# Kernel tuning notes

Hardware: AMD Instinct MI355X
Metric: run time of the kernel (lower is better)

Reference implementation:

```python
import jax, jax.numpy as jnp
import numpy as np

M = 100   # memory_size
D = 512   # memory_dim
B, C, H, W = 4, 512, 64, 64
LN_EPS = 512.0  # nn.LayerNorm(300, 512): 2nd positional arg is eps (faithful quirk)


def _l2norm(x):
    # F.normalize(x, dim=1): x / max(||x||_2, 1e-12)
    return x / jnp.maximum(jnp.linalg.norm(x, axis=1, keepdims=True), 1e-12)


def setup_inputs() -> dict:
    key = jax.random.key(0)
    ks = jax.random.split(key, 16)
    s = 0.03  # weight scale to keep activations sane
    return {
        "fea":    jax.random.normal(ks[0], (B, C, H, W), jnp.float32),
        "item_w": jax.random.normal(ks[1], (D, D), jnp.float32) * 0.02,
        "rel_w":  jax.random.normal(ks[2], (M, D, D), jnp.float32) * 0.02,
        "W1": jax.random.normal(ks[3], (C, D), jnp.float32) * s,  "b1": jnp.zeros((D,), jnp.float32),
        "W2": jax.random.normal(ks[4], (C, D), jnp.float32) * s,  "b2": jnp.zeros((D,), jnp.float32),
        "W3": jax.random.normal(ks[5], (C, M), jnp.float32) * s,  "b3": jnp.zeros((M,), jnp.float32),
        "Wqkv": jax.random.normal(ks[6], (D, 3 * M), jnp.float32) * s, "bqkv": jnp.zeros((3 * M,), jnp.float32),
        "ln_g": jnp.ones((3 * M,), jnp.float32), "ln_b": jnp.zeros((3 * M,), jnp.float32),
        "Wr1": jax.random.normal(ks[7], (D * D, D), jnp.float32) * s, "br1": jnp.zeros((D,), jnp.float32),
        "Wr2": jax.random.normal(ks[8], (M * D, D), jnp.float32) * s, "br2": jnp.zeros((D,), jnp.float32),
    }


def reference(fea, item_w, rel_w, W1, b1, W2, b2, W3, b3,
              Wqkv, bqkv, ln_g, ln_b, Wr1, br1, Wr2, br2):
    b, c, h, w = fea.shape
    x = fea.transpose(0, 2, 3, 1).reshape(b * h * w, c)        # (N, C)
    qn = _l2norm(x)
    ip1 = qn @ W1 + b1                                          # (N, D)
    ip2 = qn @ W2 + b2                                          # (N, D)
    ip3 = jax.nn.softmax(qn @ W3 + b3, axis=-1)                 # (N, M)
    # ip4[b,f] = sum_{n,d} ip3[b,n] ip2[b,d] rel_w[n,d,f]; scan over the M
    # memory slots to avoid an (N, M, D) intermediate.
    def _slot(acc, nw):
        coef, Wn = nw                                           # (N,), (D, D)
        return acc + coef[:, None] * (ip2 @ Wn), None
    ip4, _ = jax.lax.scan(_slot, jnp.zeros_like(ip2), (ip3.T, rel_w))
    # einsum('bd,cf->df', ip4, ip2) == outer(sum_b ip4, sum_c ip2)
    item0 = jnp.outer(ip4.sum(0), ip2.sum(0))                   # (D, D)
    item1 = item_w + ip1.T @ ip1                                # (D, D)
    qkv = (item0 + 1.0 * item1) @ Wqkv + bqkv                   # alpha2=1.0, (D, 3M)
    mu = qkv.mean(-1, keepdims=True)
    var = jnp.var(qkv, axis=-1, keepdims=True)                  # biased, as torch LN
    qkv = (qkv - mu) / jnp.sqrt(var + LN_EPS) * ln_g + ln_b
    q, k, v = qkv[:, :M].T, qkv[:, M:2 * M].T, qkv[:, 2 * M:].T  # each (M, D)
    # op_att: rel0[i,d,f] = sum_j tanh(q[i,d]*k[j,d]) * v[j,f]
    t = jnp.tanh(q[:, None, :] * k[None, :, :])                 # (M, M, D)
    rel0 = jnp.einsum('ijd,jf->idf', t, v)                      # (M, D, D)
    rel_w_new = rel_w + 1.0 * rel0                              # alpha1=1.0
    memory = rel_w_new.reshape(M, D * D) @ Wr1 + br1            # (M, D)
    mn = _l2norm(memory)
    addr = jax.nn.softmax(qn @ mn.T, axis=1)                    # (N, M)
    mf = (addr @ mn).reshape(b, h, w, c).transpose(0, 3, 1, 2)  # (b, C, h, w)
    return jnp.concatenate([fea, mf], axis=1)                   # (b, 2C, h, w)
```

## Files before the change

### kernel.cpp

```cpp
#include <hip/hip_runtime.h>
#include <hip/hip_bf16.h>

#define NTOK 16384
#define DDIM 512
#define MMEM 100
#define HWSZ 4096
#define QKVW 300

typedef __attribute__((ext_vector_type(8))) short short8v;
typedef __attribute__((ext_vector_type(4))) short short4v;
typedef __attribute__((ext_vector_type(4))) float f32x4;

__device__ __forceinline__ unsigned short f2bf(float x) {
  union { __hip_bfloat16 h; unsigned short u; } cv;
  cv.h = __float2bfloat16(x);
  return cv.u;
}
__device__ __forceinline__ float bf2f(unsigned short u) {
  union { unsigned int u; float f; } v; v.u = ((unsigned int)u) << 16;
  return v.f;
}

__global__ __launch_bounds__(256) void feat_cvtw_k(
    const float* __restrict__ fea, unsigned short* __restrict__ qnbf,
    float* __restrict__ out,
    const float* __restrict__ W1, const float* __restrict__ W2,
    const float* __restrict__ W3, const float* __restrict__ Wq,
    const float* __restrict__ b1, const float* __restrict__ b2,
    unsigned short* __restrict__ Wcat, unsigned short* __restrict__ o3,
    unsigned short* __restrict__ oq, float* __restrict__ bcat,
    float* __restrict__ zbase) {
  if (blockIdx.x >= 741) {
    int zidx = (blockIdx.x - 741) * 256 + threadIdx.x;
    if (zidx < 78592)
      ((float4*)zbase)[zidx] = make_float4(0.f, 0.f, 0.f, 0.f);
    return;
  }
  if (blockIdx.x >= 512) {
    int base = (blockIdx.x - 512) * 256 + threadIdx.x;
    for (int idx = base; idx < 467968; idx += 229 * 256) {
      if (idx < 262144) {
        int k = idx >> 9, n = idx & 511;
        Wcat[(size_t)k * 1024 + n] = f2bf(W1[idx]);
        Wcat[(size_t)k * 1024 + 512 + n] = f2bf(W2[idx]);
      } else if (idx < 313344) {
        o3[idx - 262144] = f2bf(W3[idx - 262144]);
      } else if (idx < 466944) {
        oq[idx - 313344] = f2bf(Wq[idx - 313344]);
      } else {
        int i = idx - 466944;
        bcat[i] = (i < 512) ? b1[i] : b2[i - 512];
      }
    }
    return;
  }
  __shared__ float tile[512][33];
  __shared__ float psum[8][32];
  __shared__ float invn_s[32];
  const int bid = blockIdx.x;
  const int b = bid >> 7, hw0 = (bid & 127) * 32;
  const int t = threadIdx.x;
  const int hwo = t & 31, cg = t >> 5;
  const float* src = fea + (size_t)b * DDIM * HWSZ + hw0;
  float* dst = out + (size_t)b * (2 * DDIM) * HWSZ + hw0;
  float ss = 0.f;
#pragma unroll 8
  for (int i = 0; i < 64; ++i) {
    int c = cg * 64 + i;
    float v = src[(size_t)c * HWSZ + hwo];
    tile[c][hwo] = v;
    dst[(size_t)c * HWSZ + hwo] = v;
    ss += v * v;
  }
  psum[cg][hwo] = ss;
  __syncthreads();
  if (t < 32) {
    float s = 0.f;
#pragma unroll
    for (int j = 0; j < 8; ++j) s += psum[j][t];
    invn_s[t] = 1.f / fmaxf(sqrtf(s), 1e-12f);
  }
  __syncthreads();
  const int tok = t & 31, c0 = (t >> 5) * 64;
  const float inv = invn_s[tok];
  unsigned short* qp = qnbf + ((size_t)(b * HWSZ + hw0 + tok)) * DDIM + c0;
#pragma unroll
  for (int e8 = 0; e8 < 8; ++e8) {
    short8v p;
#pragma unroll
    for (int e = 0; e < 8; ++e)
      p[e] = (short)f2bf(tile[c0 + e8 * 8 + e][tok] * inv);
    *(short8v*)(qp + e8 * 8) = p;
  }
}

__device__ __forceinline__ void gemm_body(
    char* smem, const unsigned short* __restrict__ A,
    const unsigned short* __restrict__ B, const float* __restrict__ bias,
    unsigned short* __restrict__ Cbf,
    int M, int N, int K, int lda, int ldb, int ldc, int bx, int by) {
  unsigned short (*As)[40] = (unsigned short(*)[40])smem;
  unsigned short (*Bs)[132] = (unsigned short(*)[132])(smem + 10240);
  const int tid = threadIdx.x;
  const int l = tid & 63, w = tid >> 6;
  const int l15 = l & 15, lhi = l >> 4;
  const int wm = w >> 1, wn = w & 1;
  const int row0 = by * 128, col0 = bx * 128;
  const int am = tid >> 1, akq = (tid & 1) << 4;
  const int bk = tid >> 3, bnq = (tid & 7) << 4;
  const int arow = row0 + am;
  f32x4 acc[4][4] = {};

  for (int k0 = 0; k0 < K; k0 += 32) {
    short8v av0 = {}, av1 = {}, bv0 = {}, bv1 = {};
    if (arow < M && k0 + akq < K) {
      const unsigned short* ap = A + (size_t)arow * lda + k0 + akq;
      if (k0 + akq + 15 < K) {
        av0 = *(const short8v*)ap;
        av1 = *(const short8v*)(ap + 8);
      } else {
#pragma unroll
        for (int e = 0; e < 8; ++e) {
          av0[e] = (k0 + akq + e < K) ? (short)ap[e] : (short)0;
          av1[e] = (k0 + akq + 8 + e < K) ? (short)ap[8 + e] : (short)0;
        }
      }
    }
    {
      const int kk = k0 + bk;
      if (kk < K) {
        const unsigned short* bp = B + (size_t)kk * ldb + col0 + bnq;
        if (col0 + bnq + 15 < N) {
          bv0 = *(const short8v*)bp;
          bv1 = *(const short8v*)(bp + 8);
        } else {
#pragma unroll
          for (int e = 0; e < 8; ++e) {
            bv0[e] = (col0 + bnq + e < N) ? (short)bp[e] : (short)0;
            bv1[e] = (col0 + bnq + 8 + e < N) ? (short)bp[8 + e] : (short)0;
          }
        }
      }
    }
    __syncthreads();
    *(short8v*)&As[am][akq] = av0;
    *(short8v*)&As[am][akq + 8] = av1;
    *(short8v*)&Bs[bk][bnq] = bv0;
    *(short8v*)&Bs[bk][bnq + 8] = bv1;
    __syncthreads();
    short8v af[4];
#pragma unroll
    for (int mt = 0; mt < 4; ++mt)
      af[mt] = *(const short8v*)&As[wm * 64 + mt * 16 + l15][lhi * 8];
#pragma unroll
    for (int ct = 0; ct < 4; ++ct) {
      union { short8v v; unsigned short u[8]; } bf;
      const int nn = wn * 64 + ct * 16 + l15;
#pragma unroll
      for (int j = 0; j < 8; ++j) bf.u[j] = Bs[lhi * 8 + j][nn];
#pragma unroll
      for (int mt = 0; mt < 4; ++mt)
        acc[mt][ct] = __builtin_amdgcn_mfma_f32_16x16x32_bf16(
            af[mt], bf.v, acc[mt][ct], 0, 0, 0);
    }
  }

#pragma unroll
  for (int mt = 0; mt < 4; ++mt) {
    const int rb = row0 + wm * 64 + mt * 16 + lhi * 4;
#pragma unroll
    for (int u = 0; u < 4; ++u) {
      const int r = rb + u;
      if (r >= M) continue;
#pragma unroll
      for (int ct = 0; ct < 4; ++ct) {
        const int c = col0 + wn * 64 + ct * 16 + l15;
        if (c >= N) continue;
        float val = acc[mt][ct][u];
        if (bias) val += bias[c];
        Cbf[(size_t)r * ldc + c] = f2bf(val);
      }
    }
  }
}

__device__ __forceinline__ void sm100_body(
    char* smem, const unsigned short* __restrict__ A,
    const unsigned short* __restrict__ B, const float* __restrict__ bias,
    unsigned short* __restrict__ obf, int lda, int ldb, int ldo, int rowblk) {
  unsigned short (*As)[40] = (unsigned short(*)[40])smem;
  unsigned short (*Bs)[132] = (unsigned short(*)[132])(smem + 10240);
  unsigned short (*Ps)[104] = (unsigned short(*)[104])smem;
  const int tid = threadIdx.x;
  const int l = tid & 63, w = tid >> 6;
  const int l15 = l & 15, lhi = l >> 4;
  const int wm = w >> 1, wn = w & 1;
  const int row0 = rowblk * 128;
  const int am = tid >> 1, akq = (tid & 1) << 4;
  const int bk = tid >> 3, bnq = (tid & 7) << 4;
  f32x4 acc[4][4] = {};

  for (int k0 = 0; k0 < DDIM; k0 += 32) {
    const unsigned short* ap = A + (size_t)(row0 + am) * lda + k0 + akq;
    short8v av0 = *(const short8v*)ap;
    short8v av1 = *(const short8v*)(ap + 8);
    short8v bv0 = {}, bv1 = {};
    const unsigned short* bp = B + (size_t)(k0 + bk) * ldb + bnq;
    if (bnq + 15 < MMEM) {
      bv0 = *(const short8v*)bp;
      bv1 = *(const short8v*)(bp + 8);
    } else {
#pragma unroll
      for (int e = 0; e < 8; ++e) {
        bv0[e] = (bnq + e < MMEM) ? (short)bp[e] : (short)0;
        bv1[e] = (bnq + 8 + e < MMEM) ? (short)bp[8 + e] : (short)0;
      }
    }
    __syncthreads();
    *(short8v*)&As[am][akq] = av0;
    *(short8v*)&As[am][akq + 8] = av1;
    *(short8v*)&Bs[bk][bnq] = bv0;
    *(short8v*)&Bs[bk][bnq + 8] = bv1;
    __syncthreads();
    short8v af[4];
#pragma unroll
    for (int mt = 0; mt < 4; ++mt)
      af[mt] = *(const short8v*)&As[wm * 64 + mt * 16 + l15][lhi * 8];
#pragma unroll
    for (int ct = 0; ct < 4; ++ct) {
      union { short8v v; unsigned short u[8]; } bf;
      const int nn = wn * 64 + ct * 16 + l15;
#pragma unroll
      for (int j = 0; j < 8; ++j) bf.u[j] = Bs[lhi * 8 + j][nn];
#pragma unroll
      for (int mt = 0; mt < 4; ++mt)
        acc[mt][ct] = __builtin_amdgcn_mfma_f32_16x16x32_bf16(
            af[mt], bf.v, acc[mt][ct], 0, 0, 0);
    }
  }

  __syncthreads();
#pragma unroll
  for (int mt = 0; mt < 4; ++mt) {
#pragma unroll
    for (int u = 0; u < 4; ++u) {
      const int r = wm * 64 + mt * 16 + lhi * 4 + u;
#pragma unroll
      for (int ct = 0; ct < 4; ++ct) {
        const int c = wn * 64 + ct * 16 + l15;
        if (c < MMEM) {
          float val = acc[mt][ct][u];
          if (bias) val += bias[c];
          Ps[r][c] = f2bf(val);
        }
      }
    }
  }
  __syncthreads();
  for (int rr = 0; rr < 32; ++rr) {
    const int r = w * 32 + rr;
    float v0 = bf2f(Ps[r][l]);
    const bool has1 = (l + 64) < MMEM;
    float v1 = has1 ? bf2f(Ps[r][l + 64]) : -3.4e38f;
    float m = fmaxf(v0, v1);
#pragma unroll
    for (int o = 32; o; o >>= 1) m = fmaxf(m, __shfl_xor(m, o, 64));
    float e0 = expf(v0 - m);
    float e1 = has1 ? expf(v1 - m) : 0.f;
    float s = e0 + e1;
#pragma unroll
    for (int o = 32; o; o >>= 1) s += __shfl_xor(s, o, 64);
    float inv = 1.f / s;
    unsigned short* orow = obf + (size_t)(row0 + r) * ldo;
    orow[l] = f2bf(e0 * inv);
    if (has1) orow[l + 64] = f2bf(e1 * inv);
  }
}

__device__ __forceinline__ void atb_body(
    char* smem, const unsigned short* __restrict__ A,
    const unsigned short* __restrict__ B, float* __restrict__ C,
    int M, int N, int K, int lda, int ldb, int ldc, int KC,
    int bx, int by, int bz) {
  unsigned short (*As)[40] = (unsigned short(*)[40])smem;
  unsigned short (*Bs)[132] = (unsigned short(*)[132])(smem + 10240);
  const int tid = threadIdx.x;
  const int l = tid & 63, w = tid >> 6;
  const int l15 = l & 15, lhi = l >> 4;
  const int wm = w >> 1, wn = w & 1;
  const int row0 = by * 128, col0 = bx * 128;
  const int kbeg = bz * KC;
  const int kend = min(kbeg + KC, K);
  const int akk = tid >> 3, amq = (tid & 7) << 4;
  const int bk = tid >> 3, bnq = (tid & 7) << 4;
  f32x4 acc[4][4] = {};

  for (int k0 = kbeg; k0 < kend; k0 += 32) {
    unsigned short av[16]; short8v bv0 = {}, bv1 = {};
    {
      const int kk = k0 + akk;
      if (kk < kend) {
        const unsigned short* ap = A + (size_t)kk * lda + row0 + amq;
        if (row0 + amq + 15 < M) {
          *(short8v*)&av[0] = *(const short8v*)ap;
          *(short8v*)&av[8] = *(const short8v*)(ap + 8);
        } else {
#pragma unroll
          for (int e = 0; e < 16; ++e)
            av[e] = (row0 + amq + e < M) ? ap[e] : 0;
        }
      } else {
#pragma unroll
        for (int e = 0; e < 16; ++e) av[e] = 0;
      }
    }
    {
      const int kk = k0 + bk;
      if (kk < kend) {
        const unsigned short* bp = B + (size_t)kk * ldb + col0 + bnq;
        if (col0 + bnq + 15 < N) {
          bv0 = *(const short8v*)bp;
          bv1 = *(const short8v*)(bp + 8);
        } else {
#pragma unroll
          for (int e = 0; e < 8; ++e) {
            bv0[e] = (col0 + bnq + e < N) ? (short)bp[e] : (short)0;
            bv1[e] = (col0 + bnq + 8 + e < N) ? (short)bp[8 + e] : (short)0;
          }
        }
      }
    }
    __syncthreads();
#pragma unroll
    for (int e = 0; e < 16; ++e) As[amq + e][akk] = av[e];
    *(short8v*)&Bs[bk][bnq] = bv0;
    *(short8v*)&Bs[bk][bnq + 8] = bv1;
    __syncthreads();
    short8v af[4];
#pragma unroll
    for (int mt = 0; mt < 4; ++mt)
      af[mt] = *(const short8v*)&As[wm * 64 + mt * 16 + l15][lhi * 8];
#pragma unroll
    for (int ct = 0; ct < 4; ++ct) {
      union { short8v v; unsigned short u[8]; } bf;
      const int nn = wn * 64 + ct * 16 + l15;
#pragma unroll
      for (int j = 0; j < 8; ++j) bf.u[j] = Bs[lhi * 8 + j][nn];
#pragma unroll
      for (int mt = 0; mt < 4; ++mt)
        acc[mt][ct] = __builtin_amdgcn_mfma_f32_16x16x32_bf16(
            af[mt], bf.v, acc[mt][ct], 0, 0, 0);
    }
  }

#pragma unroll
  for (int mt = 0; mt < 4; ++mt) {
    const int rb = row0 + wm * 64 + mt * 16 + lhi * 4;
#pragma unroll
    for (int u = 0; u < 4; ++u) {
      const int r = rb + u;
      if (r >= M) continue;
#pragma unroll
      for (int ct = 0; ct < 4; ++ct) {
        const int c = col0 + wn * 64 + ct * 16 + l15;
        if (c >= N) continue;
        atomicAdd(&C[(size_t)r * ldc + c], acc[mt][ct][u]);
      }
    }
  }
}

__global__ __launch_bounds__(256) void step2_k(
    const unsigned short* __restrict__ qnbf, const unsigned short* __restrict__ Wcat,
    const float* __restrict__ bcat, unsigned short* __restrict__ ip12bf,
    const unsigned short* __restrict__ W3bf, const float* __restrict__ b3,
    unsigned short* __restrict__ ip3bf) {
  __shared__ char smem[26624];
  const int bid = blockIdx.x;
  if (bid < 1024) {
    gemm_body(smem, qnbf, Wcat, bcat, ip12bf, NTOK, 1024, DDIM,
              DDIM, 1024, 1024, bid & 7, bid >> 3);
  } else {
    sm100_body(smem, qnbf, W3bf, b3, ip3bf, DDIM, MMEM, MMEM, bid - 1024);
  }
}

__global__ __launch_bounds__(256) void step3_k(
    const unsigned short* __restrict__ ip12bf, const unsigned short* __restrict__ ip3bf,
    float* __restrict__ item, float* __restrict__ S, float* __restrict__ ip2sum) {
  __shared__ char smem[18688];
  const int bid = blockIdx.x;
  const int t = threadIdx.x;
  if (bid < 512) {
    atb_body(smem, ip12bf, ip12bf, item, DDIM, DDIM, NTOK,
             1024, 1024, DDIM, 512, bid & 3, (bid >> 2) & 3, bid >> 4);
  } else if (bid < 768) {
    const int b2 = bid - 512;
    atb_body(smem, ip3bf, ip12bf + 512, S, MMEM, DDIM, NTOK,
             MMEM, 1024, DDIM, 256, b2 & 3, 0, b2 >> 2);
  } else {
    const int cb = bid - 768;
    const unsigned short* p = ip12bf + 512 + (size_t)cb * 64 * 1024 + t;
    float a0 = 0.f, a1 = 0.f, a2 = 0.f, a3 = 0.f;
    float b0 = 0.f, b1 = 0.f, b2 = 0.f, b3 = 0.f;
    for (int r = 0; r < 64; r += 4) {
      a0 += bf2f(p[(size_t)(r + 0) * 1024]); b0 += bf2f(p[(size_t)(r + 0) * 1024 + 256]);
      a1 += bf2f(p[(size_t)(r + 1) * 1024]); b1 += bf2f(p[(size_t)(r + 1) * 1024 + 256]);
      a2 += bf2f(p[(size_t)(r + 2) * 1024]); b2 += bf2f(p[(size_t)(r + 2) * 1024 + 256]);
      a3 += bf2f(p[(size_t)(r + 3) * 1024]); b3 += bf2f(p[(size_t)(r + 3) * 1024 + 256]);
    }
    atomicAdd(&ip2sum[t], (a0 + a1) + (a2 + a3));
    atomicAdd(&ip2sum[t + 256], (b0 + b1) + (b2 + b3));
  }
}

__global__ __launch_bounds__(256) void sm100_addr_k(
    const unsigned short* __restrict__ qnbf, const unsigned short* __restrict__ mnTbf,
    unsigned short* __restrict__ addrbf) {
  __shared__ char smem[26624];
  sm100_body(smem, qnbf, mnTbf, nullptr, addrbf, DDIM, MMEM, 128, blockIdx.x);
}

__global__ __launch_bounds__(256) void gemm_mf_out_k(
    const unsigned short* __restrict__ A, const unsigned short* __restrict__ B,
    float* __restrict__ out) {
  __shared__ char smem[35328];
  unsigned short (*As)[40] = (unsigned short(*)[40])smem;
  unsigned short (*Bs)[132] = (unsigned short(*)[132])(smem + 10240);
  unsigned short (*Ps)[138] = (unsigned short(*)[138])smem;
  const int tid = threadIdx.x;
  const int l = tid & 63, w = tid >> 6;
  const int l15 = l & 15, lhi = l >> 4;
  const int wm = w >> 1, wn = w & 1;
  const int row0 = blockIdx.y * 128, col0 = blockIdx.x * 128;
  const int am = tid >> 1, akq = (tid & 1) << 4;
  const int bk = tid >> 3, bnq = (tid & 7) << 4;
  const int K = MMEM, lda = 128, ldb = DDIM;
  f32x4 acc[4][4] = {};

  for (int k0 = 0; k0 < 128; k0 += 32) {
    short8v av0 = {}, av1 = {}, bv0 = {}, bv1 = {};
    if (k0 + akq < K) {
      const unsigned short* ap = A + (size_t)(row0 + am) * lda + k0 + akq;
      if (k0 + akq + 15 < K) {
        av0 = *(const short8v*)ap;
        av1 = *(const short8v*)(ap + 8);
      } else {
#pragma unroll
        for (int e = 0; e < 8; ++e) {
          av0[e] = (k0 + akq + e < K) ? (short)ap[e] : (short)0;
          av1[e] = (k0 + akq + 8 + e < K) ? (short)ap[8 + e] : (short)0;
        }
      }
    }
    {
      const int kk = k0 + bk;
      if (kk < K) {
        const unsigned short* bp = B + (size_t)kk * ldb + col0 + bnq;
        bv0 = *(const short8v*)bp;
        bv1 = *(const short8v*)(bp + 8);
      }
    }
    __syncthreads();
    *(short8v*)&As[am][akq] = av0;
    *(short8v*)&As[am][akq + 8] = av1;
    *(short8v*)&Bs[bk][bnq] = bv0;
    *(short8v*)&Bs[bk][bnq + 8] = bv1;
    __syncthreads();
    short8v af[4];
#pragma unroll
    for (int mt = 0; mt < 4; ++mt)
      af[mt] = *(const short8v*)&As[wm * 64 + mt * 16 + l15][lhi * 8];
#pragma unroll
    for (int ct = 0; ct < 4; ++ct) {
      union { short8v v; unsigned short u[8]; } bf;
      const int nn = wn * 64 + ct * 16 + l15;
#pragma unroll
      for (int j = 0; j < 8; ++j) bf.u[j] = Bs[lhi * 8 + j][nn];
#pragma unroll
      for (int mt = 0; mt < 4; ++mt)
        acc[mt][ct] = __builtin_amdgcn_mfma_f32_16x16x32_bf16(
            af[mt], bf.v, acc[mt][ct], 0, 0, 0);
    }
  }

  __syncthreads();
#pragma unroll
  for (int mt = 0; mt < 4; ++mt) {
#pragma unroll
    for (int u = 0; u < 4; ++u) {
      const int r = wm * 64 + mt * 16 + lhi * 4 + u;
#pragma unroll
      for (int ct = 0; ct < 4; ++ct) {
        const int c = wn * 64 + ct * 16 + l15;
        Ps[r][c] = f2bf(acc[mt][ct][u]);
      }
    }
  }
  __syncthreads();
  const int b = row0 >> 12;
  const int hwb = row0 & 4095;
  const int j = tid & 63;
  float* obase = out + (size_t)b * 4194304 + (size_t)(512 + col0) * HWSZ + hwb;
  for (int cr = tid >> 6; cr < 128; cr += 4) {
    obase[(size_t)cr * HWSZ + j]      = bf2f(Ps[j][cr]);
    obase[(size_t)cr * HWSZ + j + 64] = bf2f(Ps[j + 64][cr]);
  }
}

__global__ __launch_bounds__(256) void gemm_qkv_k(
    const float* __restrict__ item, const float* __restrict__ item_w,
    const float* __restrict__ s4, const float* __restrict__ s2,
    const unsigned short* __restrict__ B, const float* __restrict__ bias,
    float* __restrict__ C) {
  __shared__ unsigned short As[128][40];
  __shared__ unsigned short Bs[32][132];
  const int tid = threadIdx.x;
  const int l = tid & 63, w = tid >> 6;
  const int l15 = l & 15, lhi = l >> 4;
  const int wm = w >> 1, wn = w & 1;
  const int row0 = blockIdx.y * 128, col0 = blockIdx.x * 128;
  const int am = tid >> 1, akq = (tid & 1) << 4;
  const int bk = tid >> 3, bnq = (tid & 7) << 4;
  const int arow = row0 + am;
  f32x4 acc[4][4] = {};

  for (int k0 = 0; k0 < DDIM; k0 += 32) {
    float av[16];
    {
      const size_t off = (size_t)arow * DDIM + k0 + akq;
      const float s4r = s4[arow];
#pragma unroll
      for (int u = 0; u < 4; ++u) {
        float4 a = *(const float4*)(item + off + 4 * u);
        float4 b = *(const float4*)(item_w + off + 4 * u);
        float4 c = *(const float4*)(s2 + k0 + akq + 4 * u);
        av[4*u+0] = a.x + b.x + s4r * c.x;
        av[4*u+1] = a.y + b.y + s4r * c.y;
        av[4*u+2] = a.z + b.z + s4r * c.z;
        av[4*u+3] = a.w + b.w + s4r * c.w;
      }
    }
    short8v bv0 = {}, bv1 = {};
    {
      const int kk = k0 + bk;
      const unsigned short* bp = B + (size_t)kk * QKVW + col0 + bnq;
      if (col0 + bnq + 15 < QKVW) {
        bv0 = *(const short8v*)bp;
        bv1 = *(const short8v*)(bp + 8);
      } else {
#pragma unroll
        for (int e = 0; e < 8; ++e) {
          bv0[e] = (col0 + bnq + e < QKVW) ? (short)bp[e] : (short)0;
          bv1[e] = (col0 + bnq + 8 + e < QKVW) ? (short)bp[8 + e] : (short)0;
        }
      }
    }
    __syncthreads();
    {
      short8v p0, p1;
#pragma unroll
      for (int e = 0; e < 8; ++e) p0[e] = (short)f2bf(av[e]);
#pragma unroll
      for (int e = 0; e < 8; ++e) p1[e] = (short)f2bf(av[8 + e]);
      *(short8v*)&As[am][akq] = p0;
      *(short8v*)&As[am][akq + 8] = p1;
    }
    *(short8v*)&Bs[bk][bnq] = bv0;
    *(short8v*)&Bs[bk][bnq + 8] = bv1;
    __syncthreads();
    short8v af[4];
#pragma unroll
    for (int mt = 0; mt < 4; ++mt)
      af[mt] = *(const short8v*)&As[wm * 64 + mt * 16 + l15][lhi * 8];
#pragma unroll
    for (int ct = 0; ct < 4; ++ct) {
      union { short8v v; unsigned short u[8]; } bf;
      const int nn = wn * 64 + ct * 16 + l15;
#pragma unroll
      for (int j = 0; j < 8; ++j) bf.u[j] = Bs[lhi * 8 + j][nn];
#pragma unroll
      for (int mt = 0; mt < 4; ++mt)
        acc[mt][ct] = __builtin_amdgcn_mfma_f32_16x16x32_bf16(
            af[mt], bf.v, acc[mt][ct], 0, 0, 0);
    }
  }

#pragma unroll
  for (int mt = 0; mt < 4; ++mt) {
    const int rb = row0 + wm * 64 + mt * 16 + lhi * 4;
#pragma unroll
    for (int u = 0; u < 4; ++u) {
      const int r = rb + u;
#pragma unroll
      for (int ct = 0; ct < 4; ++ct) {
        const int c = col0 + wn * 64 + ct * 16 + l15;
        if (c >= QKVW) continue;
        C[(size_t)r * QKVW + c] = acc[mt][ct][u] + bias[c];
      }
    }
  }
}

__global__ __launch_bounds__(256) void rel0_mfma_k(
    const float* __restrict__ qm, const float* __restrict__ km,
    const float* __restrict__ vm, const float* __restrict__ rel_w,
    unsigned short* __restrict__ relbf) {
  __shared__ unsigned short Ts[128][136];
  __shared__ unsigned short Vs[128][136];
  __shared__ float qv[128];
  const int i = blockIdx.y;
  const int d0 = blockIdx.x * 128;
  const int tid = threadIdx.x;
  const int l = tid & 63, w = tid >> 6;
  const int l15 = l & 15, lhi = l >> 4;
  const int wm = w >> 1, wn = w & 1;

  if (tid < 128) qv[tid] = qm[(size_t)i * DDIM + d0 + tid];
  __syncthreads();
#pragma unroll
  for (int p = 0; p < 8; ++p) {
    int g = p * 2048 + tid * 8;
    int j = g >> 7, dd = g & 127;
    if (j < MMEM) {
      const float* kp = km + (size_t)j * DDIM + d0 + dd;
      float4 k0v = *(const float4*)kp;
      float4 k1v = *(const float4*)(kp + 4);
      float kv[8] = {k0v.x, k0v.y, k0v.z, k0v.w, k1v.x, k1v.y, k1v.z, k1v.w};
#pragma unroll
      for (int e = 0; e < 8; ++e)
        Ts[dd + e][j] = f2bf(tanhf(qv[dd + e] * kv[e]));
    } else {
#pragma unroll
      for (int e = 0; e < 8; ++e) Ts[dd + e][j] = 0;
    }
  }

  for (int f0 = 0; f0 < DDIM; f0 += 128) {
    __syncthreads();
#pragma unroll
    for (int p = 0; p < 8; ++p) {
      int g = p * 2048 + tid * 8;
      int j = g >> 7, ff = g & 127;
      short8v pv;
      if (j < MMEM) {
        const float* vp = vm + (size_t)j * DDIM + f0 + ff;
        float4 v0 = *(const float4*)vp;
        float4 v1 = *(const float4*)(vp + 4);
        pv[0] = (short)f2bf(v0.x); pv[1] = (short)f2bf(v0.y);
        pv[2] = (short)f2bf(v0.z); pv[3] = (short)f2bf(v0.w);
        pv[4] = (short)f2bf(v1.x); pv[5] = (short)f2bf(v1.y);
        pv[6] = (short)f2bf(v1.z); pv[7] = (short)f2bf(v1.w);
      } else {
#pragma unroll
        for (int e = 0; e < 8; ++e) pv[e] = 0;
      }
      *(short8v*)&Vs[j][ff] = pv;
    }
    __syncthreads();
    f32x4 acc[4][4] = {};
#pragma unroll
    for (int ks = 0; ks < 4; ++ks) {
      const int kb = ks * 32;
      short8v af[4];
#pragma unroll
      for (int mt = 0; mt < 4; ++mt)
        af[mt] = *(const short8v*)&Ts[wm * 64 + mt * 16 + l15][kb + lhi * 8];
#pragma unroll
      for (int ct = 0; ct < 4; ++ct) {
        union { short8v v; unsigned short u[8]; } bf;
        const int nn = wn * 64 + ct * 16 + l15;
#pragma unroll
        for (int jj = 0; jj < 8; ++jj) bf.u[jj] = Vs[kb + lhi * 8 + jj][nn];
#pragma unroll
        for (int mt = 0; mt < 4; ++mt)
          acc[mt][ct] = __builtin_amdgcn_mfma_f32_16x16x32_bf16(
              af[mt], bf.v, acc[mt][ct], 0, 0, 0);
      }
    }
#pragma unroll
    for (int mt = 0; mt < 4; ++mt) {
#pragma unroll
      for (int u = 0; u < 4; ++u) {
        const int d = d0 + wm * 64 + mt * 16 + lhi * 4 + u;
        const size_t base = (size_t)i * 262144 + (size_t)d * DDIM;
#pragma unroll
        for (int ct = 0; ct < 4; ++ct) {
          const int f = f0 + wn * 64 + ct * 16 + l15;
          relbf[base + f] = f2bf(rel_w[base + f] + acc[mt][ct][u]);
        }
      }
    }
  }
}

#define MGK 262144
#define MGKC 1024
#define MGCHUNK 256
__global__ __launch_bounds__(1024, 4) void memgemm_k(
    const unsigned short* __restrict__ Ag, const float* __restrict__ Bg,
    unsigned short* __restrict__ partial) {
  __shared__ unsigned short As[128][44];
  __shared__ unsigned short Bs[32][520];
  const int tid = threadIdx.x;
  const int l = tid & 63, w = tid >> 6;
  const int l15 = l & 15, lhi = l >> 4;
  const int kbeg = blockIdx.x * MGKC;
  const int arow = tid >> 3, akq = tid & 7;
  const int bk = tid >> 5, bnq = (tid & 31) * 16;
  const int bsw = ((bk >> 3) & 3) << 4;
  const int csw = lhi << 4;
  f32x4 acc[8][2] = {};

  for (int t32 = 0; t32 < MGKC / 32; ++t32) {
    const int kb = kbeg + t32 * 32;
    short4v av = {};
    if (arow < MMEM)
      av = *(const short4v*)(Ag + (size_t)arow * MGK + kb + akq * 4);
    float4 bv[4];
    const float* bp = Bg + (size_t)(kb + bk) * DDIM + bnq;
#pragma unroll
    for (int u = 0; u < 4; ++u) bv[u] = *(const float4*)(bp + 4 * u);
    __syncthreads();
    *(short4v*)&As[arow][akq * 4] = av;
#pragma unroll
    for (int u = 0; u < 2; ++u) {
      short8v pb;
      pb[0] = (short)f2bf(bv[2*u].x);   pb[1] = (short)f2bf(bv[2*u].y);
      pb[2] = (short)f2bf(bv[2*u].z);   pb[3] = (short)f2bf(bv[2*u].w);
      pb[4] = (short)f2bf(bv[2*u+1].x); pb[5] = (short)f2bf(bv[2*u+1].y);
      pb[6] = (short)f2bf(bv[2*u+1].z); pb[7] = (short)f2bf(bv[2*u+1].w);
      *(short8v*)&Bs[bk][(bnq + u * 8) ^ bsw] = pb;
    }
    __syncthreads();
    union { short8v v; unsigned short u[8]; } bf0, bf1;
    const int nn0 = w * 32 + l15, nn1 = w * 32 + 16 + l15;
#pragma unroll
    for (int j = 0; j < 8; ++j) {
      bf0.u[j] = Bs[lhi * 8 + j][nn0 ^ csw];
      bf1.u[j] = Bs[lhi * 8 + j][nn1 ^ csw];
    }
#pragma unroll
    for (int mt = 0; mt < 8; ++mt) {
      short8v af = *(const short8v*)&As[mt * 16 + l15][lhi * 8];
      acc[mt][0] = __builtin_amdgcn_mfma_f32_16x16x32_bf16(af, bf0.v, acc[mt][0], 0, 0, 0);
      acc[mt][1] = __builtin_amdgcn_mfma_f32_16x16x32_bf16(af, bf1.v, acc[mt][1], 0, 0, 0);
    }
  }

  unsigned short* pw = partial + (size_t)blockIdx.x * (MMEM * DDIM);
#pragma unroll
  for (int mt = 0; mt < 8; ++mt) {
    const int r0 = mt * 16 + lhi * 4;
#pragma unroll
    for (int r = 0; r < 4; ++r) {
      const int row = r0 + r;
      if (row < MMEM) {
        pw[(size_t)row * DDIM + w * 32 + l15]      = f2bf(acc[mt][0][r]);
        pw[(size_t)row * DDIM + w * 32 + 16 + l15] = f2bf(acc[mt][1][r]);
      }
    }
  }
}

__global__ __launch_bounds__(512) void reduce_mn_k(
    const unsigned short* __restrict__ partial, const float* __restrict__ br1,
    unsigned short* __restrict__ mnbf, unsigned short* __restrict__ mnTbf) {
  __shared__ float r1[8];
  const int i = blockIdx.x, t = threadIdx.x;
  const unsigned short* p = partial + (size_t)i * DDIM + t;
  float a[16] = {};
  const size_t zs = (size_t)(MMEM * DDIM);
  for (int z = 0; z < MGCHUNK; z += 16) {
#pragma unroll
    for (int e = 0; e < 16; ++e) a[e] += bf2f(p[(z + e) * zs]);
  }
  float s = br1[t];
#pragma unroll
  for (int e = 0; e < 16; ++e) s += a[e];
  float q = s * s;
#pragma unroll
  for (int o = 32; o; o >>= 1) q += __shfl_xor(q, o, 64);
  if ((t & 63) == 0) r1[t >> 6] = q;
  __syncthreads();
  q = 0.f;
#pragma unroll
  for (int j = 0; j < 8; ++j) q += r1[j];
  float inv = 1.f / fmaxf(sqrtf(q), 1e-12f);
  unsigned short hv = f2bf(s * inv);
  mnbf[(size_t)i * DDIM + t] = hv;
  mnTbf[(size_t)t * MMEM + i] = hv;
}

__global__ __launch_bounds__(256) void ip4sum_k(const float* __restrict__ S,
                                                const float* __restrict__ rel_w,
                                                float* __restrict__ out) {
  __shared__ float sv[64];
  int r0 = blockIdx.x * 64;
  int tid = threadIdx.x;
  if (tid < 64) sv[tid] = S[r0 + tid];
  __syncthreads();
  float a0 = 0.f, a1 = 0.f, a2 = 0.f, a3 = 0.f;
  float b0 = 0.f, b1 = 0.f, b2 = 0.f, b3 = 0.f;
  const float* base = rel_w + (size_t)r0 * DDIM;
  for (int r = 0; r < 64; r += 4) {
    const float* p0 = base + (size_t)(r + 0) * DDIM;
    const float* p1 = base + (size_t)(r + 1) * DDIM;
    const float* p2 = base + (size_t)(r + 2) * DDIM;
    const float* p3 = base + (size_t)(r + 3) * DDIM;
    a0 = fmaf(sv[r + 0], p0[tid], a0); b0 = fmaf(sv[r + 0], p0[tid + 256], b0);
    a1 = fmaf(sv[r + 1], p1[tid], a1); b1 = fmaf(sv[r + 1], p1[tid + 256], b1);
    a2 = fmaf(sv[r + 2], p2[tid], a2); b2 = fmaf(sv[r + 2], p2[tid + 256], b2);
    a3 = fmaf(sv[r + 3], p3[tid], a3); b3 = fmaf(sv[r + 3], p3[tid + 256], b3);
  }
  atomicAdd(&out[tid], (a0 + a1) + (a2 + a3));
  atomicAdd(&out[tid + 256], (b0 + b1) + (b2 + b3));
}

__global__ __launch_bounds__(256) void ln300_k(const float* __restrict__ x,
                                               const float* __restrict__ g,
                                               const float* __restrict__ bb,
                                               float* __restrict__ qm,
                                               float* __restrict__ km,
                                               float* __restrict__ vm) {
  __shared__ float r1[4], r2[4];
  int row = blockIdx.x, tid = threadIdx.x;
  const float* xr = x + (size_t)row * QKVW;
  float v1 = xr[tid];
  float v2 = (tid + 256 < QKVW) ? xr[tid + 256] : 0.f;
  float s = v1 + v2, q = v1 * v1 + v2 * v2;
#pragma unroll
  for (int o = 32; o; o >>= 1) { s += __shfl_xor(s, o, 64); q += __shfl_xor(q, o, 64); }
  if ((tid & 63) == 0) { r1[tid >> 6] = s; r2[tid >> 6] = q; }
  __syncthreads();
  s = r1[0] + r1[1] + r1[2] + r1[3];
  q = r2[0] + r2[1] + r2[2] + r2[3];
  float mean = s * (1.f / 300.f);
  float var = q * (1.f / 300.f) - mean * mean;
  float inv = rsqrtf(var + 512.0f);
  float y1 = (v1 - mean) * inv * g[tid] + bb[tid];
  int j = tid;
  if (j < 100)      qm[(size_t)j * DDIM + row] = y1;
  else if (j < 200) km[(size_t)(j - 100) * DDIM + row] = y1;
  else              vm[(size_t)(j - 200) * DDIM + row] = y1;
  if (tid + 256 < QKVW) {
    float y2 = (v2 - mean) * inv * g[tid + 256] + bb[tid + 256];
    vm[(size_t)(tid + 56) * DDIM + row] = y2;
  }
}

extern "C" void kernel_launch(void* const* d_in, const int* in_sizes, int n_in,
                              void* d_out, int out_size, void* d_ws, size_t ws_size,
                              hipStream_t stream) {
  (void)in_sizes; (void)n_in; (void)out_size; (void)ws_size;
  const float* fea    = (const float*)d_in[0];
  const float* item_w = (const float*)d_in[1];
  const float* rel_w  = (const float*)d_in[2];
  const float* W1     = (const float*)d_in[3];
  const float* b1     = (const float*)d_in[4];
  const float* W2     = (const float*)d_in[5];
  const float* b2     = (const float*)d_in[6];
  const float* W3     = (const float*)d_in[7];
  const float* b3     = (const float*)d_in[8];
  const float* Wqkv   = (const float*)d_in[9];
  const float* bqkv   = (const float*)d_in[10];
  const float* ln_g   = (const float*)d_in[11];
  const float* ln_b   = (const float*)d_in[12];
  const float* Wr1    = (const float*)d_in[13];
  const float* br1    = (const float*)d_in[14];
  float* out = (float*)d_out;
  float* ws = (float*)d_ws;

  float* S       = ws;
  float* ip4sum  = S       + 51200;
  float* ip2sum  = ip4sum  + 512;
  float* item    = ip2sum  + 512;
  float* qkv     = item    + 262144;
  float* qm      = qkv     + 153600;
  float* km      = qm      + 51200;
  float* vm      = km      + 51200;
  float* bcat    = vm      + 51200;
  unsigned short* u16base = (unsigned short*)(bcat + 1024);
  unsigned short* partial = u16base;
  unsigned short* qnbf    = partial + 13107200;
  unsigned short* ip12bf  = qnbf    + 8388608;
  unsigned short* ip3bf   = ip12bf  + 16777216;
  unsigned short* addrbf  = ip3bf   + 1638400;
  unsigned short* relbf   = addrbf  + 2097152;
  unsigned short* mnbf    = relbf   + 26214400;
  unsigned short* mnTbf   = mnbf    + 51200;
  unsigned short* Wcat    = mnTbf   + 51200;
  unsigned short* W3bf    = Wcat    + 524288;
  unsigned short* Wqbf    = W3bf    + 51200;

  feat_cvtw_k<<<1048, 256, 0, stream>>>(fea, qnbf, out, W1, W2, W3, Wqkv,
                                        b1, b2, Wcat, W3bf, Wqbf, bcat, S);

  step2_k<<<1152, 256, 0, stream>>>(qnbf, Wcat, bcat, ip12bf, W3bf, b3, ip3bf);

  step3_k<<<1024, 256, 0, stream>>>(ip12bf, ip3bf, item, S, ip2sum);

  ip4sum_k<<<800, 256, 0, stream>>>(S, rel_w, ip4sum);

  gemm_qkv_k<<<dim3(3, 4), 256, 0, stream>>>(item, item_w, ip4sum, ip2sum,
                                             Wqbf, bqkv, qkv);
  ln300_k<<<512, 256, 0, stream>>>(qkv, ln_g, ln_b, qm, km, vm);

  rel0_mfma_k<<<dim3(4, MMEM), 256, 0, stream>>>(qm, km, vm, rel_w, relbf);

  memgemm_k<<<dim3(MGCHUNK), 1024, 0, stream>>>(relbf, Wr1, partial);
  reduce_mn_k<<<MMEM, 512, 0, stream>>>(partial, br1, mnbf, mnTbf);

  sm100_addr_k<<<128, 256, 0, stream>>>(qnbf, mnTbf, addrbf);
  gemm_mf_out_k<<<dim3(4, 128), 256, 0, stream>>>(addrbf, mnbf, out);
}
```

Baseline: 485.9 us.

## Exploit Gram symmetry and fold rank-one qkv term into LayerNorm, merging kernels

The ip1ᵀip1 Gram product now computes only the upper-triangle 128x128 tiles (10 of 16) and mirrors off-diagonal results with a second atomic add. The rank-one outer(ip4sum, ip2sum) term is taken out of the qkv GEMM input. It is applied after the GEMM as ip4sum[row]*(ip2sum·Wqkv), with that vector computed in fp32 by one block. This lets the ip4sum reduction and the qkv GEMM run in a single merged launch instead of two dependent ones. The cost is doubled atomics on off-diagonal tiles, a serial 512x300 dot-product block, and a rank-one term that is no longer rounded to bf16.

Result: slower. 542.4 us (+11.6%).

```diff
diff --git a/kernel.cpp b/kernel.cpp
--- a/kernel.cpp
+++ b/kernel.cpp
@@ -281,7 +281,7 @@
     char* smem, const unsigned short* __restrict__ A,
     const unsigned short* __restrict__ B, float* __restrict__ C,
     int M, int N, int K, int lda, int ldb, int ldc, int KC,
-    int bx, int by, int bz) {
+    int bx, int by, int bz, bool mirror) {
   unsigned short (*As)[40] = (unsigned short(*)[40])smem;
   unsigned short (*Bs)[132] = (unsigned short(*)[132])(smem + 10240);
   const int tid = threadIdx.x;
@@ -365,6 +365,7 @@
         const int c = col0 + wn * 64 + ct * 16 + l15;
         if (c >= N) continue;
         atomicAdd(&C[(size_t)r * ldc + c], acc[mt][ct][u]);
+        if (mirror) atomicAdd(&C[(size_t)c * ldc + r], acc[mt][ct][u]);
       }
     }
   }
@@ -391,15 +392,18 @@
   __shared__ char smem[18688];
   const int bid = blockIdx.x;
   const int t = threadIdx.x;
-  if (bid < 512) {
+  if (bid < 320) {
+    const int tabx[10] = {0, 1, 2, 3, 1, 2, 3, 2, 3, 3};
+    const int taby[10] = {0, 1, 2, 3, 0, 0, 0, 1, 1, 2};
+    const int p = bid >> 5, bz = bid & 31;
     atb_body(smem, ip12bf, ip12bf, item, DDIM, DDIM, NTOK,
-             1024, 1024, DDIM, 512, bid & 3, (bid >> 2) & 3, bid >> 4);
-  } else if (bid < 768) {
-    const int b2 = bid - 512;
+             1024, 1024, DDIM, 512, tabx[p], taby[p], bz, tabx[p] != taby[p]);
+  } else if (bid < 576) {
+    const int b2 = bid - 320;
     atb_body(smem, ip3bf, ip12bf + 512, S, MMEM, DDIM, NTOK,
-             MMEM, 1024, DDIM, 256, b2 & 3, 0, b2 >> 2);
+             MMEM, 1024, DDIM, 256, b2 & 3, 0, b2 >> 2, false);
   } else {
-    const int cb = bid - 768;
+    const int cb = bid - 576;
     const unsigned short* p = ip12bf + 512 + (size_t)cb * 64 * 1024 + t;
     float a0 = 0.f, a1 = 0.f, a2 = 0.f, a3 = 0.f;
     float b0 = 0.f, b1 = 0.f, b2 = 0.f, b3 = 0.f;
@@ -411,6 +415,137 @@
     }
     atomicAdd(&ip2sum[t], (a0 + a1) + (a2 + a3));
     atomicAdd(&ip2sum[t + 256], (b0 + b1) + (b2 + b3));
+  }
+}
+
+__global__ __launch_bounds__(256) void step4_k(
+    const float* __restrict__ S, const float* __restrict__ rel_w,
+    float* __restrict__ ip4sum,
+    const float* __restrict__ item, const float* __restrict__ item_w,
+    const unsigned short* __restrict__ Wqbf, const float* __restrict__ bqkv,
+    float* __restrict__ qkv,
+    const float* __restrict__ ip2sum, const float* __restrict__ Wqkv,
+    float* __restrict__ t2) {
+  __shared__ char smem[18688];
+  const int bid = blockIdx.x;
+  const int tid = threadIdx.x;
+  if (bid < 800) {
+    float* sv = (float*)smem;
+    int r0 = bid * 64;
+    if (tid < 64) sv[tid] = S[r0 + tid];
+    __syncthreads();
+    float a0 = 0.f, a1 = 0.f, a2 = 0.f, a3 = 0.f;
+    float b0 = 0.f, b1 = 0.f, b2 = 0.f, b3 = 0.f;
+    const float* base = rel_w + (size_t)r0 * DDIM;
+    for (int r = 0; r < 64; r += 4) {
+      const float* p0 = base + (size_t)(r + 0) * DDIM;
+      const float* p1 = base + (size_t)(r + 1) * DDIM;
+      const float* p2 = base + (size_t)(r + 2) * DDIM;
+      const float* p3 = base + (size_t)(r + 3) * DDIM;
+      a0 = fmaf(sv[r + 0], p0[tid], a0); b0 = fmaf(sv[r + 0], p0[tid + 256], b0);
+      a1 = fmaf(sv[r + 1], p1[tid], a1); b1 = fmaf(sv[r + 1], p1[tid + 256], b1);
+      a2 = fmaf(sv[r + 2], p2[tid], a2); b2 = fmaf(sv[r + 2], p2[tid + 256], b2);
+      a3 = fmaf(sv[r + 3], p3[tid], a3); b3 = fmaf(sv[r + 3], p3[tid + 256], b3);
+    }
+    atomicAdd(&ip4sum[tid], (a0 + a1) + (a2 + a3));
+    atomicAdd(&ip4sum[tid + 256], (b0 + b1) + (b2 + b3));
+    return;
+  }
+  if (bid == 812) {
+    for (int n = tid; n < QKVW; n += 256) {
+      float s = 0.f;
+      for (int d = 0; d < DDIM; ++d) s = fmaf(ip2sum[d], Wqkv[(size_t)d * QKVW + n], s);
+      t2[n] = s;
+    }
+    return;
+  }
+  {
+    unsigned short (*As)[40] = (unsigned short(*)[40])smem;
+    unsigned short (*Bs)[132] = (unsigned short(*)[132])(smem + 10240);
+    const int qb = bid - 800;
+    const int bx = qb % 3, by = qb / 3;
+    const int l = tid & 63, w = tid >> 6;
+    const int l15 = l & 15, lhi = l >> 4;
+    const int wm = w >> 1, wn = w & 1;
+    const int row0 = by * 128, col0 = bx * 128;
+    const int am = tid >> 1, akq = (tid & 1) << 4;
+    const int bk = tid >> 3, bnq = (tid & 7) << 4;
+    const int arow = row0 + am;
+    f32x4 acc[4][4] = {};
+
+    for (int k0 = 0; k0 < DDIM; k0 += 32) {
+      float av[16];
+      {
+        const size_t off = (size_t)arow * DDIM + k0 + akq;
+#pragma unroll
+        for (int u = 0; u < 4; ++u) {
+          float4 a = *(const float4*)(item + off + 4 * u);
+          float4 b = *(const float4*)(item_w + off + 4 * u);
+          av[4*u+0] = a.x + b.x;
+          av[4*u+1] = a.y + b.y;
+          av[4*u+2] = a.z + b.z;
+          av[4*u+3] = a.w + b.w;
+        }
+      }
+      short8v bv0 = {}, bv1 = {};
+      {
+        const int kk = k0 + bk;
+        const unsigned short* bp = Wqbf + (size_t)kk * QKVW + col0 + bnq;
+        if (col0 + bnq + 15 < QKVW) {
+          bv0 = *(const short8v*)bp;
+          bv1 = *(const short8v*)(bp + 8);
+        } else {
+#pragma unroll
+          for (int e = 0; e < 8; ++e) {
+            bv0[e] = (col0 + bnq + e < QKVW) ? (short)bp[e] : (short)0;
+            bv1[e] = (col0 + bnq + 8 + e < QKVW) ? (short)bp[8 + e] : (short)0;
+          }
+        }
+      }
+      __syncthreads();
+      {
+        short8v p0, p1;
+#pragma unroll
+        for (int e = 0; e < 8; ++e) p0[e] = (short)f2bf(av[e]);
+#pragma unroll
+        for (int e = 0; e < 8; ++e) p1[e] = (short)f2bf(av[8 + e]);
+        *(short8v*)&As[am][akq] = p0;
+        *(short8v*)&As[am][akq + 8] = p1;
+      }
+      *(short8v*)&Bs[bk][bnq] = bv0;
+      *(short8v*)&Bs[bk][bnq + 8] = bv1;
+      __syncthreads();
+      short8v af[4];
+#pragma unroll
+      for (int mt = 0; mt < 4; ++mt)
+        af[mt] = *(const short8v*)&As[wm * 64 + mt * 16 + l15][lhi * 8];
+#pragma unroll
+      for (int ct = 0; ct < 4; ++ct) {
+        union { short8v v; unsigned short u[8]; } bf;
+        const int nn = wn * 64 + ct * 16 + l15;
+#pragma unroll
+        for (int j = 0; j < 8; ++j) bf.u[j] = Bs[lhi * 8 + j][nn];
+#pragma unroll
+        for (int mt = 0; mt < 4; ++mt)
+          acc[mt][ct] = __builtin_amdgcn_mfma_f32_16x16x32_bf16(
+              af[mt], bf.v, acc[mt][ct], 0, 0, 0);
+      }
+    }
+
+#pragma unroll
+    for (int mt = 0; mt < 4; ++mt) {
+      const int rb = row0 + wm * 64 + mt * 16 + lhi * 4;
+#pragma unroll
+      for (int u = 0; u < 4; ++u) {
+        const int r = rb + u;
+#pragma unroll
+        for (int ct = 0; ct < 4; ++ct) {
+          const int c = col0 + wn * 64 + ct * 16 + l15;
+          if (c >= QKVW) continue;
+          qkv[(size_t)r * QKVW + c] = acc[mt][ct][u] + bqkv[c];
+        }
+      }
+    }
   }
 }
 
@@ -505,100 +640,6 @@
   for (int cr = tid >> 6; cr < 128; cr += 4) {
     obase[(size_t)cr * HWSZ + j]      = bf2f(Ps[j][cr]);
     obase[(size_t)cr * HWSZ + j + 64] = bf2f(Ps[j + 64][cr]);
-  }
-}
-
-__global__ __launch_bounds__(256) void gemm_qkv_k(
-    const float* __restrict__ item, const float* __restrict__ item_w,
-    const float* __restrict__ s4, const float* __restrict__ s2,
-    const unsigned short* __restrict__ B, const float* __restrict__ bias,
-    float* __restrict__ C) {
-  __shared__ unsigned short As[128][40];
-  __shared__ unsigned short Bs[32][132];
-  const int tid = threadIdx.x;
-  const int l = tid & 63, w = tid >> 6;
-  const int l15 = l & 15, lhi = l >> 4;
-  const int wm = w >> 1, wn = w & 1;
-  const int row0 = blockIdx.y * 128, col0 = blockIdx.x * 128;
-  const int am = tid >> 1, akq = (tid & 1) << 4;
-  const int bk = tid >> 3, bnq = (tid & 7) << 4;
-  const int arow = row0 + am;
-  f32x4 acc[4][4] = {};
-
-  for (int k0 = 0; k0 < DDIM; k0 += 32) {
-    float av[16];
-    {
-      const size_t off = (size_t)arow * DDIM + k0 + akq;
-      const float s4r = s4[arow];
-#pragma unroll
-      for (int u = 0; u < 4; ++u) {
-        float4 a = *(const float4*)(item + off + 4 * u);
-        float4 b = *(const float4*)(item_w + off + 4 * u);
-        float4 c = *(const float4*)(s2 + k0 + akq + 4 * u);
-        av[4*u+0] = a.x + b.x + s4r * c.x;
-        av[4*u+1] = a.y + b.y + s4r * c.y;
-        av[4*u+2] = a.z + b.z + s4r * c.z;
-        av[4*u+3] = a.w + b.w + s4r * c.w;
-      }
-    }
-    short8v bv0 = {}, bv1 = {};
-    {
-      const int kk = k0 + bk;
-      const unsigned short* bp = B + (size_t)kk * QKVW + col0 + bnq;
-      if (col0 + bnq + 15 < QKVW) {
-        bv0 = *(const short8v*)bp;
-        bv1 = *(const short8v*)(bp + 8);
-      } else {
-#pragma unroll
-        for (int e = 0; e < 8; ++e) {
-          bv0[e] = (col0 + bnq + e < QKVW) ? (short)bp[e] : (short)0;
-          bv1[e] = (col0 + bnq + 8 + e < QKVW) ? (short)bp[8 + e] : (short)0;
-        }
-      }
-    }
-    __syncthreads();
-    {
-      short8v p0, p1;
-#pragma unroll
-      for (int e = 0; e < 8; ++e) p0[e] = (short)f2bf(av[e]);
-#pragma unroll
-      for (int e = 0; e < 8; ++e) p1[e] = (short)f2bf(av[8 + e]);
-      *(short8v*)&As[am][akq] = p0;
-      *(short8v*)&As[am][akq + 8] = p1;
-    }
-    *(short8v*)&Bs[bk][bnq] = bv0;
-    *(short8v*)&Bs[bk][bnq + 8] = bv1;
-    __syncthreads();
-    short8v af[4];
-#pragma unroll
-    for (int mt = 0; mt < 4; ++mt)
-      af[mt] = *(const short8v*)&As[wm * 64 + mt * 16 + l15][lhi * 8];
-#pragma unroll
-    for (int ct = 0; ct < 4; ++ct) {
-      union { short8v v; unsigned short u[8]; } bf;
-      const int nn = wn * 64 + ct * 16 + l15;
-#pragma unroll
-      for (int j = 0; j < 8; ++j) bf.u[j] = Bs[lhi * 8 + j][nn];
-#pragma unroll
-      for (int mt = 0; mt < 4; ++mt)
-        acc[mt][ct] = __builtin_amdgcn_mfma_f32_16x16x32_bf16(
-            af[mt], bf.v, acc[mt][ct], 0, 0, 0);
-    }
-  }
-
-#pragma unroll
-  for (int mt = 0; mt < 4; ++mt) {
-    const int rb = row0 + wm * 64 + mt * 16 + lhi * 4;
-#pragma unroll
-    for (int u = 0; u < 4; ++u) {
-      const int r = rb + u;
-#pragma unroll
-      for (int ct = 0; ct < 4; ++ct) {
-        const int c = col0 + wn * 64 + ct * 16 + l15;
-        if (c >= QKVW) continue;
-        C[(size_t)r * QKVW + c] = acc[mt][ct][u] + bias[c];
-      }
-    }
   }
 }
 
@@ -792,32 +833,9 @@
   mnTbf[(size_t)t * MMEM + i] = hv;
 }
 
-__global__ __launch_bounds__(256) void ip4sum_k(const float* __restrict__ S,
-                                                const float* __restrict__ rel_w,
-                                                float* __restrict__ out) {
-  __shared__ float sv[64];
-  int r0 = blockIdx.x * 64;
-  int tid = threadIdx.x;
-  if (tid < 64) sv[tid] = S[r0 + tid];
-  __syncthreads();
-  float a0 = 0.f, a1 = 0.f, a2 = 0.f, a3 = 0.f;
-  float b0 = 0.f, b1 = 0.f, b2 = 0.f, b3 = 0.f;
-  const float* base = rel_w + (size_t)r0 * DDIM;
-  for (int r = 0; r < 64; r += 4) {
-    const float* p0 = base + (size_t)(r + 0) * DDIM;
-    const float* p1 = base + (size_t)(r + 1) * DDIM;
-    const float* p2 = base + (size_t)(r + 2) * DDIM;
-    const float* p3 = base + (size_t)(r + 3) * DDIM;
-    a0 = fmaf(sv[r + 0], p0[tid], a0); b0 = fmaf(sv[r + 0], p0[tid + 256], b0);
-    a1 = fmaf(sv[r + 1], p1[tid], a1); b1 = fmaf(sv[r + 1], p1[tid + 256], b1);
-    a2 = fmaf(sv[r + 2], p2[tid], a2); b2 = fmaf(sv[r + 2], p2[tid + 256], b2);
-    a3 = fmaf(sv[r + 3], p3[tid], a3); b3 = fmaf(sv[r + 3], p3[tid + 256], b3);
-  }
-  atomicAdd(&out[tid], (a0 + a1) + (a2 + a3));
-  atomicAdd(&out[tid + 256], (b0 + b1) + (b2 + b3));
-}
-
 __global__ __launch_bounds__(256) void ln300_k(const float* __restrict__ x,
+                                               const float* __restrict__ s4,
+                                               const float* __restrict__ t2,
                                                const float* __restrict__ g,
                                                const float* __restrict__ bb,
                                                float* __restrict__ qm,
@@ -826,8 +844,9 @@
   __shared__ float r1[4], r2[4];
   int row = blockIdx.x, tid = threadIdx.x;
   const float* xr = x + (size_t)row * QKVW;
-  float v1 = xr[tid];
-  float v2 = (tid + 256 < QKVW) ? xr[tid + 256] : 0.f;
+  const float s4r = s4[row];
+  float v1 = xr[tid] + s4r * t2[tid];
+  float v2 = (tid + 256 < QKVW) ? (xr[tid + 256] + s4r * t2[tid + 256]) : 0.f;
   float s = v1 + v2, q = v1 * v1 + v2 * v2;
 #pragma unroll
   for (int o = 32; o; o >>= 1) { s += __shfl_xor(s, o, 64); q += __shfl_xor(q, o, 64); }
@@ -880,7 +899,8 @@
   float* km      = qm      + 51200;
   float* vm      = km      + 51200;
   float* bcat    = vm      + 51200;
-  unsigned short* u16base = (unsigned short*)(bcat + 1024);
+  float* t2      = bcat    + 1024;
+  unsigned short* u16base = (unsigned short*)(t2 + 512);
   unsigned short* partial = u16base;
   unsigned short* qnbf    = partial + 13107200;
   unsigned short* ip12bf  = qnbf    + 8388608;
@@ -898,13 +918,12 @@
 
   step2_k<<<1152, 256, 0, stream>>>(qnbf, Wcat, bcat, ip12bf, W3bf, b3, ip3bf);
 
-  step3_k<<<1024, 256, 0, stream>>>(ip12bf, ip3bf, item, S, ip2sum);
-
-  ip4sum_k<<<800, 256, 0, stream>>>(S, rel_w, ip4sum);
-
-  gemm_qkv_k<<<dim3(3, 4), 256, 0, stream>>>(item, item_w, ip4sum, ip2sum,
-                                             Wqbf, bqkv, qkv);
-  ln300_k<<<512, 256, 0, stream>>>(qkv, ln_g, ln_b, qm, km, vm);
+  step3_k<<<832, 256, 0, stream>>>(ip12bf, ip3bf, item, S, ip2sum);
+
+  step4_k<<<813, 256, 0, stream>>>(S, rel_w, ip4sum, item, item_w,
+                                   Wqbf, bqkv, qkv, ip2sum, Wqkv, t2);
+
+  ln300_k<<<512, 256, 0, stream>>>(qkv, ip4sum, t2, ln_g, ln_b, qm, km, vm);
 
   rel0_mfma_k<<<dim3(4, MMEM), 256, 0, stream>>>(qm, km, vm, rel_w, relbf);
 
```
